# Kernel optimization log

Hardware: AMD Instinct MI355X
Metric: run time of the kernel (lower is better)

Reference implementation:

```python
import jax, jax.numpy as jnp
import numpy as np

N_NODES = 40000
N_EDGES = 300000
EMBED = 256
LN_EPS = 1e-5
LEAKY_SLOPE = 0.01


def setup_inputs() -> dict:
    key = jax.random.key(0)
    ks = jax.random.split(key, 5)
    H = jax.random.normal(ks[0], (N_NODES, EMBED), dtype=jnp.float32)
    E = jax.random.normal(ks[1], (N_EDGES, EMBED), dtype=jnp.float32)
    ht = jax.random.randint(ks[2], (N_EDGES, 2), 0, N_NODES, dtype=jnp.int64)
    # Linear weights in torch convention: [out_features, in_features]
    W_fwd = jax.random.normal(ks[3], (EMBED, 2 * EMBED), dtype=jnp.float32) * (1.0 / np.sqrt(2 * EMBED))
    W_back = jax.random.normal(ks[4], (EMBED, 2 * EMBED), dtype=jnp.float32) * (1.0 / np.sqrt(2 * EMBED))
    return {
        "H": H,
        "E": E,
        "ht": ht,
        "queries": jnp.zeros((1,), jnp.float32),            # unused (message_weighting_function=None)
        "influence_weights": jnp.zeros((1,), jnp.float32),  # modeled as None
        "W_fwd": W_fwd,
        "b_fwd": jnp.zeros((EMBED,), jnp.float32),
        "W_back": W_back,
        "b_back": jnp.zeros((EMBED,), jnp.float32),
        "ln_w": jnp.ones((EMBED,), jnp.float32),
        "ln_b": jnp.zeros((EMBED,), jnp.float32),
    }


def _layer_norm(x, w, b):
    mu = jnp.mean(x, axis=-1, keepdims=True)
    var = jnp.mean(jnp.square(x - mu), axis=-1, keepdims=True)  # biased, as torch LayerNorm
    return (x - mu) * jax.lax.rsqrt(var + LN_EPS) * w + b


def reference(H, E, ht, queries, influence_weights, W_fwd, b_fwd, W_back, b_back, ln_w, ln_b):
    # queries / influence_weights are None in the modeled configuration; ignored.
    heads = ht[:, 0]
    tails = ht[:, 1]
    n = H.shape[0]
    # gather -> concat -> linear (messages in both edge directions)
    msg_fwd = jnp.concatenate([H[heads], E], axis=1) @ W_fwd.T + b_fwd    # [m, d]
    msg_back = jnp.concatenate([H[tails], E], axis=1) @ W_back.T + b_back  # [m, d]
    # scatter-add aggregate: fwd messages go to tails, back messages to heads
    msg_dst = jnp.concatenate([tails, heads], axis=0)          # [2m]
    messages = jnp.concatenate([msg_fwd, msg_back], axis=0)    # [2m, d]
    agg = jax.ops.segment_sum(messages, msg_dst, num_segments=n)  # [n, d]
    counts = jax.ops.segment_sum(jnp.ones_like(msg_dst, dtype=H.dtype), msg_dst, num_segments=n)
    agg = agg / counts[:, None]
    out = _layer_norm(jax.nn.leaky_relu(agg, LEAKY_SLOPE) + H, ln_w, ln_b)
    return out
```

## Files before the change

kernel.cpp:

```cpp
#include <hip/hip_runtime.h>
#include <hip/hip_bf16.h>

#define N_NODES 40000
#define N_EDGES 300000
#define EMBED 256
#define CAP 64

typedef __attribute__((ext_vector_type(8))) short s16x8;
typedef __attribute__((ext_vector_type(4))) float f32x4;

__device__ __forceinline__ float b2f(unsigned short u) {
    union { unsigned int i; float f; } v; v.i = ((unsigned int)u) << 16; return v.f;
}
__device__ __forceinline__ unsigned short f2b(float f) {
    unsigned int x = __float_as_uint(f);
    x += 0x7fffu + ((x >> 16) & 1u);
    return (unsigned short)(x >> 16);
}
__device__ __forceinline__ bool ht_is_i64(const int* __restrict__ ht) {
    int o = 0;
    #pragma unroll
    for (int k = 1; k < 16; k += 2) o |= ht[k];
    return o == 0;
}
__device__ __forceinline__ int clampN(int v) {
    unsigned u = (unsigned)v;
    return (u < N_NODES) ? v : 0;
}

__global__ __launch_bounds__(256) void convert_kernel(
    const float* __restrict__ H, const float* __restrict__ Wf,
    const float* __restrict__ Wb,
    unsigned short* __restrict__ Hbf, unsigned short* __restrict__ Wcat)
{
    constexpr int NH4 = (N_NODES * EMBED) / 4;
    constexpr int NW4 = (EMBED * 2 * EMBED) / 4;
    int ci = blockIdx.x * 256 + threadIdx.x;
    const float* src; unsigned short* dst;
    if (ci < NH4) {
        src = &H[(size_t)ci * 4]; dst = &Hbf[(size_t)ci * 4];
    } else if (ci < NH4 + NW4) {
        int j = (ci - NH4) * 4; int n = j >> 9, k = j & 511;
        src = &Wf[j]; dst = &Wcat[(size_t)n * 1024 + k];
    } else if (ci < NH4 + 2 * NW4) {
        int j = (ci - NH4 - NW4) * 4; int n = j >> 9, k = j & 511;
        src = &Wb[j]; dst = &Wcat[(size_t)n * 1024 + 512 + k];
    } else return;
    float4 v = *(const float4*)src;
    ushort4 o; o.x = f2b(v.x); o.y = f2b(v.y); o.z = f2b(v.z); o.w = f2b(v.w);
    *(ushort4*)dst = o;
}

__global__ __launch_bounds__(256) void build_kernel(
    const int* __restrict__ ht,
    int* __restrict__ cntf, int* __restrict__ cntb,
    int* __restrict__ listf, int* __restrict__ listb)
{
    int e = blockIdx.x * 256 + threadIdx.x;
    if (e >= N_EDGES) return;
    const bool wide = ht_is_i64(ht);
    int head = clampN(wide ? ht[(size_t)4 * e]     : ht[2 * e]);
    int tail = clampN(wide ? ht[(size_t)4 * e + 2] : ht[2 * e + 1]);
    int pf = atomicAdd(&cntf[tail], 1);
    if (pf < CAP) listf[tail * CAP + pf] = e;
    int pb = atomicAdd(&cntb[head], 1);
    if (pb < CAP) listb[head * CAP + pb] = e;
}

__global__ __launch_bounds__(256, 4) void fused_kernel(
    const unsigned short* __restrict__ Hbf, const float* __restrict__ E,
    const int* __restrict__ ht, const unsigned short* __restrict__ Wcat,
    const float* __restrict__ bf_, const float* __restrict__ bb_,
    const float* __restrict__ H, const float* __restrict__ lw,
    const float* __restrict__ lb,
    const int* __restrict__ cntf, const int* __restrict__ cntb,
    const int* __restrict__ listf, const int* __restrict__ listb,
    float* __restrict__ out)
{
    constexpr int LDK = 1032;
    __shared__ unsigned short S[16 * LDK];
    __shared__ float stats[16][4][2];

    const int tid  = threadIdx.x;
    const int wid  = tid >> 6;
    const int lane = tid & 63;
    const int q    = lane >> 4;
    const int c    = lane & 15;
    const int m0   = blockIdx.x * 16;
    const bool wide = ht_is_i64(ht);

    int cF[4], cB[4];
    int eF[4], eB[4], nF[4], nB[4];
    #pragma unroll
    for (int i = 0; i < 4; i++) {
        const int node = m0 + wid * 4 + i;
        cF[i] = min(cntf[node], CAP);
        cB[i] = min(cntb[node], CAP);
    }
    #pragma unroll
    for (int i = 0; i < 4; i++) {
        const int node = m0 + wid * 4 + i;
        eF[i] = (lane < cF[i]) ? listf[node * CAP + lane] : 0;
        eB[i] = (lane < cB[i]) ? listb[node * CAP + lane] : 0;
    }
    #pragma unroll
    for (int i = 0; i < 4; i++) {
        nF[i] = clampN(wide ? ht[(size_t)4 * eF[i]]     : ht[2 * eF[i]]);
        nB[i] = clampN(wide ? ht[(size_t)4 * eB[i] + 2] : ht[2 * eB[i] + 1]);
    }

    const int loff = lane * 4;

    #pragma unroll
    for (int i = 0; i < 4; i++) {
        const int r = wid * 4 + i;
        float aHf[4] = {0.f,0.f,0.f,0.f}, aEf[4] = {0.f,0.f,0.f,0.f};
        float aHb[4] = {0.f,0.f,0.f,0.f}, aEb[4] = {0.f,0.f,0.f,0.f};

        for (int t = 0; t < cF[i]; t += 8) {
            float4 ev[8]; ushort4 hv[8]; float w[8];
            #pragma unroll
            for (int u = 0; u < 8; u++) {
                const int e  = __builtin_amdgcn_readlane(eF[i], t + u);
                const int nb = __builtin_amdgcn_readlane(nF[i], t + u);
                w[u] = (t + u < cF[i]) ? 1.0f : 0.0f;
                ev[u] = *(const float4*)(&E[(size_t)e * EMBED + loff]);
                hv[u] = *(const ushort4*)(&Hbf[(size_t)nb * EMBED + loff]);
            }
            #pragma unroll
            for (int u = 0; u < 8; u++) {
                aEf[0] += w[u] * ev[u].x; aEf[1] += w[u] * ev[u].y;
                aEf[2] += w[u] * ev[u].z; aEf[3] += w[u] * ev[u].w;
                aHf[0] += w[u] * b2f(hv[u].x); aHf[1] += w[u] * b2f(hv[u].y);
                aHf[2] += w[u] * b2f(hv[u].z); aHf[3] += w[u] * b2f(hv[u].w);
            }
        }
        for (int t = 0; t < cB[i]; t += 8) {
            float4 ev[8]; ushort4 hv[8]; float w[8];
            #pragma unroll
            for (int u = 0; u < 8; u++) {
                const int e  = __builtin_amdgcn_readlane(eB[i], t + u);
                const int nb = __builtin_amdgcn_readlane(nB[i], t + u);
                w[u] = (t + u < cB[i]) ? 1.0f : 0.0f;
                ev[u] = *(const float4*)(&E[(size_t)e * EMBED + loff]);
                hv[u] = *(const ushort4*)(&Hbf[(size_t)nb * EMBED + loff]);
            }
            #pragma unroll
            for (int u = 0; u < 8; u++) {
                aEb[0] += w[u] * ev[u].x; aEb[1] += w[u] * ev[u].y;
                aEb[2] += w[u] * ev[u].z; aEb[3] += w[u] * ev[u].w;
                aHb[0] += w[u] * b2f(hv[u].x); aHb[1] += w[u] * b2f(hv[u].y);
                aHb[2] += w[u] * b2f(hv[u].z); aHb[3] += w[u] * b2f(hv[u].w);
            }
        }

        ushort4 o;
        o.x=f2b(aHf[0]); o.y=f2b(aHf[1]); o.z=f2b(aHf[2]); o.w=f2b(aHf[3]);
        *(ushort4*)(&S[r * LDK +   0 + loff]) = o;
        o.x=f2b(aEf[0]); o.y=f2b(aEf[1]); o.z=f2b(aEf[2]); o.w=f2b(aEf[3]);
        *(ushort4*)(&S[r * LDK + 256 + loff]) = o;
        o.x=f2b(aHb[0]); o.y=f2b(aHb[1]); o.z=f2b(aHb[2]); o.w=f2b(aHb[3]);
        *(ushort4*)(&S[r * LDK + 512 + loff]) = o;
        o.x=f2b(aEb[0]); o.y=f2b(aEb[1]); o.z=f2b(aEb[2]); o.w=f2b(aEb[3]);
        *(ushort4*)(&S[r * LDK + 768 + loff]) = o;
    }
    __syncthreads();

    const int n0 = wid * 64;
    f32x4 acc[4];
    #pragma unroll
    for (int nt = 0; nt < 4; nt++) acc[nt] = (f32x4){0.f,0.f,0.f,0.f};

    #pragma unroll 4
    for (int k0 = 0; k0 < 1024; k0 += 32) {
        s16x8 a = *(const s16x8*)(&S[c * LDK + k0 + q * 8]);
        #pragma unroll
        for (int nt = 0; nt < 4; nt++) {
            s16x8 b = *(const s16x8*)(&Wcat[(size_t)(n0 + nt * 16 + c) * 1024 + k0 + q * 8]);
            acc[nt] = __builtin_amdgcn_mfma_f32_16x16x32_bf16(a, b, acc[nt], 0, 0, 0);
        }
    }

    float x[4][4];
    float sr[4], ssr[4];
    #pragma unroll
    for (int reg = 0; reg < 4; reg++) {
        const int row  = q * 4 + reg;
        const int node = m0 + row;
        const float cf = (float)cntf[node];
        const float cb = (float)cntb[node];
        const float tot = cf + cb;
        const float inv = (tot > 0.f) ? (1.0f / tot) : 0.f;
        float s = 0.f, ss = 0.f;
        #pragma unroll
        for (int nt = 0; nt < 4; nt++) {
            const int j = n0 + nt * 16 + c;
            float v = acc[nt][reg] + cf * bf_[j] + cb * bb_[j];
            float m = v * inv;
            m = (m > 0.f) ? m : 0.01f * m;
            float xx = m + H[(size_t)node * EMBED + j];
            x[reg][nt] = xx; s += xx; ss += xx * xx;
        }
        sr[reg] = s; ssr[reg] = ss;
    }
    #pragma unroll
    for (int off = 1; off < 16; off <<= 1) {
        #pragma unroll
        for (int reg = 0; reg < 4; reg++) {
            sr[reg]  += __shfl_xor(sr[reg],  off);
            ssr[reg] += __shfl_xor(ssr[reg], off);
        }
    }
    if (c == 0) {
        #pragma unroll
        for (int reg = 0; reg < 4; reg++) {
            stats[q * 4 + reg][wid][0] = sr[reg];
            stats[q * 4 + reg][wid][1] = ssr[reg];
        }
    }
    __syncthreads();
    #pragma unroll
    for (int reg = 0; reg < 4; reg++) {
        const int row  = q * 4 + reg;
        const int node = m0 + row;
        float s  = stats[row][0][0] + stats[row][1][0] + stats[row][2][0] + stats[row][3][0];
        float ss = stats[row][0][1] + stats[row][1][1] + stats[row][2][1] + stats[row][3][1];
        const float mean = s * (1.0f / EMBED);
        float var = ss * (1.0f / EMBED) - mean * mean;
        var = var < 0.f ? 0.f : var;
        const float rstd = rsqrtf(var + 1e-5f);
        #pragma unroll
        for (int nt = 0; nt < 4; nt++) {
            const int j = n0 + nt * 16 + c;
            out[(size_t)node * EMBED + j] = (x[reg][nt] - mean) * rstd * lw[j] + lb[j];
        }
    }
}

extern "C" void kernel_launch(void* const* d_in, const int* in_sizes, int n_in,
                              void* d_out, int out_size, void* d_ws, size_t ws_size,
                              hipStream_t stream) {
    const float* H   = (const float*)d_in[0];
    const float* E   = (const float*)d_in[1];
    const int*   ht  = (const int*)d_in[2];
    const float* Wf  = (const float*)d_in[5];
    const float* bf_ = (const float*)d_in[6];
    const float* Wb  = (const float*)d_in[7];
    const float* bb_ = (const float*)d_in[8];
    const float* lw  = (const float*)d_in[9];
    const float* lb  = (const float*)d_in[10];
    float* out = (float*)d_out;

    int* cntf  = (int*)d_ws;
    int* cntb  = cntf + 40960;
    int* listf = cntb + 40960;
    int* listb = listf + N_NODES * CAP;
    unsigned short* Hbf  = (unsigned short*)(listb + N_NODES * CAP);
    unsigned short* Wcat = Hbf + (size_t)N_NODES * EMBED;

    hipMemsetAsync(d_ws, 0, 2 * 40960 * sizeof(int), stream);

    constexpr int NCHUNK = (N_NODES * EMBED + 2 * EMBED * 2 * EMBED) / 4;
    convert_kernel<<<(NCHUNK + 255) / 256, 256, 0, stream>>>(H, Wf, Wb, Hbf, Wcat);
    build_kernel<<<(N_EDGES + 255) / 256, 256, 0, stream>>>(ht, cntf, cntb, listf, listb);
    fused_kernel<<<N_NODES / 16, 256, 0, stream>>>(Hbf, E, ht, Wcat, bf_, bb_,
                                                   H, lw, lb, cntf, cntb,
                                                   listf, listb, out);
}
```

Before: 687.4 us.

## Convert E to fp16 and interleave forward/backward edge gathers with manual waitcnt

When the workspace is large enough, the convert kernel now also writes an fp16 copy of the edge features E. The fused kernel then gathers half the bytes per edge row. The per-node gather is restructured to issue forward and backward loads together via inline asm, with explicit vmcnt waits, to raise memory-level parallelism, and launch bounds drop to 2 waves per SIMD. The trade-off is an extra full streaming pass over E every call, plus reduced precision for the E sum.

```diff
diff --git a/kernel.cpp b/kernel.cpp
--- a/kernel.cpp
+++ b/kernel.cpp
@@ -1,5 +1,6 @@
 #include <hip/hip_runtime.h>
 #include <hip/hip_bf16.h>
+#include <hip/hip_fp16.h>
 
 #define N_NODES 40000
 #define N_EDGES 300000
@@ -8,10 +9,8 @@
 
 typedef __attribute__((ext_vector_type(8))) short s16x8;
 typedef __attribute__((ext_vector_type(4))) float f32x4;
-
-__device__ __forceinline__ float b2f(unsigned short u) {
-    union { unsigned int i; float f; } v; v.i = ((unsigned int)u) << 16; return v.f;
-}
+typedef __attribute__((ext_vector_type(2))) unsigned int u32x2;
+
 __device__ __forceinline__ unsigned short f2b(float f) {
     unsigned int x = __float_as_uint(f);
     x += 0x7fffu + ((x >> 16) & 1u);
@@ -28,27 +27,45 @@
     return (u < N_NODES) ? v : 0;
 }
 
+template<bool EF16> struct EVT;
+template<> struct EVT<true>  { using T = u32x2; };
+template<> struct EVT<false> { using T = f32x4; };
+
+template<bool EF16>
 __global__ __launch_bounds__(256) void convert_kernel(
     const float* __restrict__ H, const float* __restrict__ Wf,
-    const float* __restrict__ Wb,
-    unsigned short* __restrict__ Hbf, unsigned short* __restrict__ Wcat)
+    const float* __restrict__ Wb, const float* __restrict__ E,
+    unsigned short* __restrict__ Hbf, unsigned short* __restrict__ Wcat,
+    unsigned short* __restrict__ Ef)
 {
     constexpr int NH4 = (N_NODES * EMBED) / 4;
     constexpr int NW4 = (EMBED * 2 * EMBED) / 4;
+    constexpr int NE4 = (N_EDGES * EMBED) / 4;
     int ci = blockIdx.x * 256 + threadIdx.x;
-    const float* src; unsigned short* dst;
     if (ci < NH4) {
-        src = &H[(size_t)ci * 4]; dst = &Hbf[(size_t)ci * 4];
+        float4 v = *(const float4*)&H[(size_t)ci * 4];
+        ushort4 o; o.x=f2b(v.x); o.y=f2b(v.y); o.z=f2b(v.z); o.w=f2b(v.w);
+        *(ushort4*)&Hbf[(size_t)ci * 4] = o;
     } else if (ci < NH4 + NW4) {
         int j = (ci - NH4) * 4; int n = j >> 9, k = j & 511;
-        src = &Wf[j]; dst = &Wcat[(size_t)n * 1024 + k];
+        float4 v = *(const float4*)&Wf[j];
+        ushort4 o; o.x=f2b(v.x); o.y=f2b(v.y); o.z=f2b(v.z); o.w=f2b(v.w);
+        *(ushort4*)&Wcat[(size_t)n * 1024 + k] = o;
     } else if (ci < NH4 + 2 * NW4) {
         int j = (ci - NH4 - NW4) * 4; int n = j >> 9, k = j & 511;
-        src = &Wb[j]; dst = &Wcat[(size_t)n * 1024 + 512 + k];
-    } else return;
-    float4 v = *(const float4*)src;
-    ushort4 o; o.x = f2b(v.x); o.y = f2b(v.y); o.z = f2b(v.z); o.w = f2b(v.w);
-    *(ushort4*)dst = o;
+        float4 v = *(const float4*)&Wb[j];
+        ushort4 o; o.x=f2b(v.x); o.y=f2b(v.y); o.z=f2b(v.z); o.w=f2b(v.w);
+        *(ushort4*)&Wcat[(size_t)n * 1024 + 512 + k] = o;
+    } else if (EF16 && ci < NH4 + 2 * NW4 + NE4) {
+        size_t j = (size_t)(ci - NH4 - 2 * NW4) * 4;
+        float4 v = *(const float4*)&E[j];
+        ushort4 o;
+        o.x = __half_as_ushort(__float2half(v.x));
+        o.y = __half_as_ushort(__float2half(v.y));
+        o.z = __half_as_ushort(__float2half(v.z));
+        o.w = __half_as_ushort(__float2half(v.w));
+        *(ushort4*)&Ef[j] = o;
+    }
 }
 
 __global__ __launch_bounds__(256) void build_kernel(
@@ -67,8 +84,88 @@
     if (pb < CAP) listb[head * CAP + pb] = e;
 }
 
-__global__ __launch_bounds__(256, 4) void fused_kernel(
-    const unsigned short* __restrict__ Hbf, const float* __restrict__ E,
+template<bool EF16>
+__device__ __forceinline__ void gather_node(
+    const void* __restrict__ Ep, const unsigned short* __restrict__ Hbf,
+    int eFr, int nFr, int eBr, int nBr, int ncF, int ncB, int lane,
+    float (&aHf)[4], float (&aEf)[4], float (&aHb)[4], float (&aEb)[4])
+{
+    using EV = typename EVT<EF16>::T;
+    const int nmax = (ncF > ncB) ? ncF : ncB;
+    for (int t = 0; t < nmax; t += 8) {
+        EV evf[8], evb[8]; u32x2 hvf[8], hvb[8];
+        #pragma unroll
+        for (int u = 0; u < 8; u++) {
+            const int e_  = __builtin_amdgcn_readlane(eFr, t + u);
+            const int nb_ = __builtin_amdgcn_readlane(nFr, t + u);
+            const unsigned short* ph = Hbf + (size_t)nb_ * EMBED + lane * 4;
+            if constexpr (EF16) {
+                const unsigned short* pe = (const unsigned short*)Ep + (size_t)e_ * EMBED + lane * 4;
+                asm volatile("global_load_dwordx2 %0, %1, off" : "=v"(evf[u]) : "v"(pe));
+            } else {
+                const float* pe = (const float*)Ep + (size_t)e_ * EMBED + lane * 4;
+                asm volatile("global_load_dwordx4 %0, %1, off" : "=v"(evf[u]) : "v"(pe));
+            }
+            asm volatile("global_load_dwordx2 %0, %1, off" : "=v"(hvf[u]) : "v"(ph));
+        }
+        #pragma unroll
+        for (int u = 0; u < 8; u++) {
+            const int e_  = __builtin_amdgcn_readlane(eBr, t + u);
+            const int nb_ = __builtin_amdgcn_readlane(nBr, t + u);
+            const unsigned short* ph = Hbf + (size_t)nb_ * EMBED + lane * 4;
+            if constexpr (EF16) {
+                const unsigned short* pe = (const unsigned short*)Ep + (size_t)e_ * EMBED + lane * 4;
+                asm volatile("global_load_dwordx2 %0, %1, off" : "=v"(evb[u]) : "v"(pe));
+            } else {
+                const float* pe = (const float*)Ep + (size_t)e_ * EMBED + lane * 4;
+                asm volatile("global_load_dwordx4 %0, %1, off" : "=v"(evb[u]) : "v"(pe));
+            }
+            asm volatile("global_load_dwordx2 %0, %1, off" : "=v"(hvb[u]) : "v"(ph));
+        }
+        asm volatile("s_waitcnt vmcnt(16)" ::: "memory");
+        __builtin_amdgcn_sched_barrier(0);
+        #pragma unroll
+        for (int u = 0; u < 8; u++) {
+            const float w = (t + u < ncF) ? 1.0f : 0.0f;
+            if constexpr (EF16) {
+                aEf[0] += w * __half2float(__ushort_as_half((unsigned short)(evf[u].x & 0xffffu)));
+                aEf[1] += w * __half2float(__ushort_as_half((unsigned short)(evf[u].x >> 16)));
+                aEf[2] += w * __half2float(__ushort_as_half((unsigned short)(evf[u].y & 0xffffu)));
+                aEf[3] += w * __half2float(__ushort_as_half((unsigned short)(evf[u].y >> 16)));
+            } else {
+                aEf[0] += w * evf[u].x; aEf[1] += w * evf[u].y;
+                aEf[2] += w * evf[u].z; aEf[3] += w * evf[u].w;
+            }
+            aHf[0] += w * __uint_as_float(hvf[u].x << 16);
+            aHf[1] += w * __uint_as_float(hvf[u].x & 0xffff0000u);
+            aHf[2] += w * __uint_as_float(hvf[u].y << 16);
+            aHf[3] += w * __uint_as_float(hvf[u].y & 0xffff0000u);
+        }
+        asm volatile("s_waitcnt vmcnt(0)" ::: "memory");
+        __builtin_amdgcn_sched_barrier(0);
+        #pragma unroll
+        for (int u = 0; u < 8; u++) {
+            const float w = (t + u < ncB) ? 1.0f : 0.0f;
+            if constexpr (EF16) {
+                aEb[0] += w * __half2float(__ushort_as_half((unsigned short)(evb[u].x & 0xffffu)));
+                aEb[1] += w * __half2float(__ushort_as_half((unsigned short)(evb[u].x >> 16)));
+                aEb[2] += w * __half2float(__ushort_as_half((unsigned short)(evb[u].y & 0xffffu)));
+                aEb[3] += w * __half2float(__ushort_as_half((unsigned short)(evb[u].y >> 16)));
+            } else {
+                aEb[0] += w * evb[u].x; aEb[1] += w * evb[u].y;
+                aEb[2] += w * evb[u].z; aEb[3] += w * evb[u].w;
+            }
+            aHb[0] += w * __uint_as_float(hvb[u].x << 16);
+            aHb[1] += w * __uint_as_float(hvb[u].x & 0xffff0000u);
+            aHb[2] += w * __uint_as_float(hvb[u].y << 16);
+            aHb[3] += w * __uint_as_float(hvb[u].y & 0xffff0000u);
+        }
+    }
+}
+
+template<bool EF16>
+__global__ __launch_bounds__(256, 2) void fused_kernel(
+    const unsigned short* __restrict__ Hbf, const void* __restrict__ Ep,
     const int* __restrict__ ht, const unsigned short* __restrict__ Wcat,
     const float* __restrict__ bf_, const float* __restrict__ bb_,
     const float* __restrict__ H, const float* __restrict__ lw,
@@ -117,42 +214,10 @@
         float aHf[4] = {0.f,0.f,0.f,0.f}, aEf[4] = {0.f,0.f,0.f,0.f};
         float aHb[4] = {0.f,0.f,0.f,0.f}, aEb[4] = {0.f,0.f,0.f,0.f};
 
-        for (int t = 0; t < cF[i]; t += 8) {
-            float4 ev[8]; ushort4 hv[8]; float w[8];
-            #pragma unroll
-            for (int u = 0; u < 8; u++) {
-                const int e  = __builtin_amdgcn_readlane(eF[i], t + u);
-                const int nb = __builtin_amdgcn_readlane(nF[i], t + u);
-                w[u] = (t + u < cF[i]) ? 1.0f : 0.0f;
-                ev[u] = *(const float4*)(&E[(size_t)e * EMBED + loff]);
-                hv[u] = *(const ushort4*)(&Hbf[(size_t)nb * EMBED + loff]);
-            }
-            #pragma unroll
-            for (int u = 0; u < 8; u++) {
-                aEf[0] += w[u] * ev[u].x; aEf[1] += w[u] * ev[u].y;
-                aEf[2] += w[u] * ev[u].z; aEf[3] += w[u] * ev[u].w;
-                aHf[0] += w[u] * b2f(hv[u].x); aHf[1] += w[u] * b2f(hv[u].y);
-                aHf[2] += w[u] * b2f(hv[u].z); aHf[3] += w[u] * b2f(hv[u].w);
-            }
-        }
-        for (int t = 0; t < cB[i]; t += 8) {
-            float4 ev[8]; ushort4 hv[8]; float w[8];
-            #pragma unroll
-            for (int u = 0; u < 8; u++) {
-                const int e  = __builtin_amdgcn_readlane(eB[i], t + u);
-                const int nb = __builtin_amdgcn_readlane(nB[i], t + u);
-                w[u] = (t + u < cB[i]) ? 1.0f : 0.0f;
-                ev[u] = *(const float4*)(&E[(size_t)e * EMBED + loff]);
-                hv[u] = *(const ushort4*)(&Hbf[(size_t)nb * EMBED + loff]);
-            }
-            #pragma unroll
-            for (int u = 0; u < 8; u++) {
-                aEb[0] += w[u] * ev[u].x; aEb[1] += w[u] * ev[u].y;
-                aEb[2] += w[u] * ev[u].z; aEb[3] += w[u] * ev[u].w;
-                aHb[0] += w[u] * b2f(hv[u].x); aHb[1] += w[u] * b2f(hv[u].y);
-                aHb[2] += w[u] * b2f(hv[u].z); aHb[3] += w[u] * b2f(hv[u].w);
-            }
-        }
+        const int ncF = __builtin_amdgcn_readfirstlane(cF[i]);
+        const int ncB = __builtin_amdgcn_readfirstlane(cB[i]);
+        gather_node<EF16>(Ep, Hbf, eF[i], nF[i], eB[i], nB[i], ncF, ncB, lane,
+                          aHf, aEf, aHb, aEb);
 
         ushort4 o;
         o.x=f2b(aHf[0]); o.y=f2b(aHf[1]); o.z=f2b(aHf[2]); o.w=f2b(aHf[3]);
@@ -257,13 +322,32 @@
     int* listb = listf + N_NODES * CAP;
     unsigned short* Hbf  = (unsigned short*)(listb + N_NODES * CAP);
     unsigned short* Wcat = Hbf + (size_t)N_NODES * EMBED;
+    unsigned short* Ef   = Wcat + (size_t)256 * 1024;
+
+    const size_t need_base = (size_t)(2 * 40960) * 4 + (size_t)2 * N_NODES * CAP * 4
+                           + ((size_t)N_NODES * EMBED + (size_t)256 * 1024) * 2;
+    const size_t need_ef16 = need_base + (size_t)N_EDGES * EMBED * 2;
+    const bool ef16 = (ws_size >= need_ef16);
 
     hipMemsetAsync(d_ws, 0, 2 * 40960 * sizeof(int), stream);
 
-    constexpr int NCHUNK = (N_NODES * EMBED + 2 * EMBED * 2 * EMBED) / 4;
-    convert_kernel<<<(NCHUNK + 255) / 256, 256, 0, stream>>>(H, Wf, Wb, Hbf, Wcat);
+    constexpr int NBASE = (N_NODES * EMBED + 2 * EMBED * 2 * EMBED) / 4;
+    constexpr int NEXT  = NBASE + (N_EDGES * EMBED) / 4;
+    if (ef16) {
+        convert_kernel<true><<<(NEXT + 255) / 256, 256, 0, stream>>>(
+            H, Wf, Wb, E, Hbf, Wcat, Ef);
+    } else {
+        convert_kernel<false><<<(NBASE + 255) / 256, 256, 0, stream>>>(
+            H, Wf, Wb, E, Hbf, Wcat, Ef);
+    }
     build_kernel<<<(N_EDGES + 255) / 256, 256, 0, stream>>>(ht, cntf, cntb, listf, listb);
-    fused_kernel<<<N_NODES / 16, 256, 0, stream>>>(Hbf, E, ht, Wcat, bf_, bb_,
-                                                   H, lw, lb, cntf, cntb,
-                                                   listf, listb, out);
-}
+    if (ef16) {
+        fused_kernel<true><<<N_NODES / 16, 256, 0, stream>>>(
+            Hbf, (const void*)Ef, ht, Wcat, bf_, bb_, H, lw, lb,
+            cntf, cntb, listf, listb, out);
+    } else {
+        fused_kernel<false><<<N_NODES / 16, 256, 0, stream>>>(
+            Hbf, (const void*)E, ht, Wcat, bf_, bb_, H, lw, lb,
+            cntf, cntb, listf, listb, out);
+    }
+}
```

New measurement: 731.3 us. +6.4%, slower.

## Build CSR with prefix sum and pre-permuted fp16 edge features for contiguous gathers

Applied to the files above, without the earlier changes.

Replaces the capped per-node edge lists with a CSR built from count, prefix-scan and permute kernels. The permute kernel writes E converted to fp16 twice, once in forward-destination order and once in backward-destination order, so the fused kernel reads edge features contiguously and at half width instead of gathering fp32 rows at random. This costs an extra pass over E, two 150MB-scale fp16 writes, and a serial single-block prefix scan per direction. Launch bounds drop to 2 waves per SIMD, and the old path is kept as a fallback when the workspace is too small.

```diff
diff --git a/kernel.cpp b/kernel.cpp
--- a/kernel.cpp
+++ b/kernel.cpp
@@ -1,5 +1,6 @@
 #include <hip/hip_runtime.h>
 #include <hip/hip_bf16.h>
+#include <hip/hip_fp16.h>
 
 #define N_NODES 40000
 #define N_EDGES 300000
@@ -8,6 +9,7 @@
 
 typedef __attribute__((ext_vector_type(8))) short s16x8;
 typedef __attribute__((ext_vector_type(4))) float f32x4;
+typedef __attribute__((ext_vector_type(2))) unsigned int u32x2;
 
 __device__ __forceinline__ float b2f(unsigned short u) {
     union { unsigned int i; float f; } v; v.i = ((unsigned int)u) << 16; return v.f;
@@ -51,6 +53,251 @@
     *(ushort4*)dst = o;
 }
 
+__global__ __launch_bounds__(256) void count_kernel(
+    const int* __restrict__ ht, int* __restrict__ cntf, int* __restrict__ cntb)
+{
+    int e = blockIdx.x * 256 + threadIdx.x;
+    if (e >= N_EDGES) return;
+    const bool wide = ht_is_i64(ht);
+    int head = clampN(wide ? ht[(size_t)4 * e]     : ht[2 * e]);
+    int tail = clampN(wide ? ht[(size_t)4 * e + 2] : ht[2 * e + 1]);
+    atomicAdd(&cntf[tail], 1);
+    atomicAdd(&cntb[head], 1);
+}
+
+__global__ __launch_bounds__(256) void prefix_kernel(
+    const int* __restrict__ cntf, const int* __restrict__ cntb,
+    int* __restrict__ offsf, int* __restrict__ offsb)
+{
+    const int* cnt = (blockIdx.x == 0) ? cntf : cntb;
+    int* offs      = (blockIdx.x == 0) ? offsf : offsb;
+    __shared__ int buf[256];
+    const int tid = threadIdx.x;
+    int carry = 0;
+    for (int base = 0; base < N_NODES; base += 256) {
+        const int i = base + tid;
+        const int v = (i < N_NODES) ? cnt[i] : 0;
+        buf[tid] = v;
+        __syncthreads();
+        for (int off = 1; off < 256; off <<= 1) {
+            int t = (tid >= off) ? buf[tid - off] : 0;
+            __syncthreads();
+            buf[tid] += t;
+            __syncthreads();
+        }
+        if (i < N_NODES) offs[i] = carry + buf[tid] - v;
+        carry += buf[255];
+        __syncthreads();
+    }
+}
+
+__global__ __launch_bounds__(256) void permute_kernel(
+    const float* __restrict__ E, const int* __restrict__ ht,
+    const int* __restrict__ offsf, const int* __restrict__ offsb,
+    int* __restrict__ fillf, int* __restrict__ fillb,
+    unsigned short* __restrict__ Epf, unsigned short* __restrict__ Epb,
+    int* __restrict__ nbrf, int* __restrict__ nbrb)
+{
+    const int e = blockIdx.x * 4 + (threadIdx.x >> 6);
+    if (e >= N_EDGES) return;
+    const int lane = threadIdx.x & 63;
+    const bool wide = ht_is_i64(ht);
+    const int head = clampN(wide ? ht[(size_t)4 * e]     : ht[2 * e]);
+    const int tail = clampN(wide ? ht[(size_t)4 * e + 2] : ht[2 * e + 1]);
+    int pf = 0, pb = 0;
+    if (lane == 0) {
+        pf = atomicAdd(&fillf[tail], 1);
+        pb = atomicAdd(&fillb[head], 1);
+    }
+    pf = __shfl(pf, 0); pb = __shfl(pb, 0);
+    const int sf = offsf[tail] + pf;
+    const int sb = offsb[head] + pb;
+    if (lane == 0) { nbrf[sf] = head; nbrb[sb] = tail; }
+    float4 v = *(const float4*)&E[(size_t)e * EMBED + lane * 4];
+    ushort4 o;
+    o.x = __half_as_ushort(__float2half(v.x));
+    o.y = __half_as_ushort(__float2half(v.y));
+    o.z = __half_as_ushort(__float2half(v.z));
+    o.w = __half_as_ushort(__float2half(v.w));
+    *(ushort4*)&Epf[(size_t)sf * EMBED + lane * 4] = o;
+    *(ushort4*)&Epb[(size_t)sb * EMBED + lane * 4] = o;
+}
+
+__global__ __launch_bounds__(256, 2) void csr_fused_kernel(
+    const unsigned short* __restrict__ Hbf,
+    const unsigned short* __restrict__ Epf, const unsigned short* __restrict__ Epb,
+    const unsigned short* __restrict__ Wcat,
+    const float* __restrict__ bf_, const float* __restrict__ bb_,
+    const float* __restrict__ H, const float* __restrict__ lw,
+    const float* __restrict__ lb,
+    const int* __restrict__ cntf, const int* __restrict__ cntb,
+    const int* __restrict__ offsf, const int* __restrict__ offsb,
+    const int* __restrict__ nbrf, const int* __restrict__ nbrb,
+    float* __restrict__ out)
+{
+    constexpr int LDK = 1032;
+    __shared__ unsigned short S[16 * LDK];
+    __shared__ float stats[16][4][2];
+
+    const int tid  = threadIdx.x;
+    const int wid  = tid >> 6;
+    const int lane = tid & 63;
+    const int q    = lane >> 4;
+    const int c    = lane & 15;
+    const int m0   = blockIdx.x * 16;
+    const int loff = lane * 4;
+
+    int cF[4], cB[4], oF[4], oB[4], nF[4], nB[4];
+    #pragma unroll
+    for (int i = 0; i < 4; i++) {
+        const int node = m0 + wid * 4 + i;
+        cF[i] = min(cntf[node], CAP);
+        cB[i] = min(cntb[node], CAP);
+        oF[i] = offsf[node];
+        oB[i] = offsb[node];
+    }
+    #pragma unroll
+    for (int i = 0; i < 4; i++) {
+        nF[i] = (lane < cF[i]) ? nbrf[oF[i] + lane] : 0;
+        nB[i] = (lane < cB[i]) ? nbrb[oB[i] + lane] : 0;
+    }
+
+    #pragma unroll
+    for (int i = 0; i < 4; i++) {
+        const int r = wid * 4 + i;
+        float aHf[4] = {0,0,0,0}, aEf[4] = {0,0,0,0};
+        float aHb[4] = {0,0,0,0}, aEb[4] = {0,0,0,0};
+
+        const int ncF = __builtin_amdgcn_readfirstlane(cF[i]);
+        const int obF = __builtin_amdgcn_readfirstlane(oF[i]);
+        for (int t = 0; t < ncF; t += 8) {
+            u32x2 ev[8], hv[8];
+            #pragma unroll
+            for (int u = 0; u < 8; u++) {
+                ev[u] = *(const u32x2*)(&Epf[(size_t)(obF + t + u) * EMBED + loff]);
+                const int nb = __builtin_amdgcn_readlane(nF[i], t + u);
+                hv[u] = *(const u32x2*)(&Hbf[(size_t)nb * EMBED + loff]);
+            }
+            #pragma unroll
+            for (int u = 0; u < 8; u++) {
+                const float w = (t + u < ncF) ? 1.0f : 0.0f;
+                aEf[0] += w * __half2float(__ushort_as_half((unsigned short)(ev[u].x & 0xffffu)));
+                aEf[1] += w * __half2float(__ushort_as_half((unsigned short)(ev[u].x >> 16)));
+                aEf[2] += w * __half2float(__ushort_as_half((unsigned short)(ev[u].y & 0xffffu)));
+                aEf[3] += w * __half2float(__ushort_as_half((unsigned short)(ev[u].y >> 16)));
+                aHf[0] += w * __uint_as_float(hv[u].x << 16);
+                aHf[1] += w * __uint_as_float(hv[u].x & 0xffff0000u);
+                aHf[2] += w * __uint_as_float(hv[u].y << 16);
+                aHf[3] += w * __uint_as_float(hv[u].y & 0xffff0000u);
+            }
+        }
+        const int ncB = __builtin_amdgcn_readfirstlane(cB[i]);
+        const int obB = __builtin_amdgcn_readfirstlane(oB[i]);
+        for (int t = 0; t < ncB; t += 8) {
+            u32x2 ev[8], hv[8];
+            #pragma unroll
+            for (int u = 0; u < 8; u++) {
+                ev[u] = *(const u32x2*)(&Epb[(size_t)(obB + t + u) * EMBED + loff]);
+                const int nb = __builtin_amdgcn_readlane(nB[i], t + u);
+                hv[u] = *(const u32x2*)(&Hbf[(size_t)nb * EMBED + loff]);
+            }
+            #pragma unroll
+            for (int u = 0; u < 8; u++) {
+                const float w = (t + u < ncB) ? 1.0f : 0.0f;
+                aEb[0] += w * __half2float(__ushort_as_half((unsigned short)(ev[u].x & 0xffffu)));
+                aEb[1] += w * __half2float(__ushort_as_half((unsigned short)(ev[u].x >> 16)));
+                aEb[2] += w * __half2float(__ushort_as_half((unsigned short)(ev[u].y & 0xffffu)));
+                aEb[3] += w * __half2float(__ushort_as_half((unsigned short)(ev[u].y >> 16)));
+                aHb[0] += w * __uint_as_float(hv[u].x << 16);
+                aHb[1] += w * __uint_as_float(hv[u].x & 0xffff0000u);
+                aHb[2] += w * __uint_as_float(hv[u].y << 16);
+                aHb[3] += w * __uint_as_float(hv[u].y & 0xffff0000u);
+            }
+        }
+
+        ushort4 o;
+        o.x=f2b(aHf[0]); o.y=f2b(aHf[1]); o.z=f2b(aHf[2]); o.w=f2b(aHf[3]);
+        *(ushort4*)(&S[r * LDK +   0 + loff]) = o;
+        o.x=f2b(aEf[0]); o.y=f2b(aEf[1]); o.z=f2b(aEf[2]); o.w=f2b(aEf[3]);
+        *(ushort4*)(&S[r * LDK + 256 + loff]) = o;
+        o.x=f2b(aHb[0]); o.y=f2b(aHb[1]); o.z=f2b(aHb[2]); o.w=f2b(aHb[3]);
+        *(ushort4*)(&S[r * LDK + 512 + loff]) = o;
+        o.x=f2b(aEb[0]); o.y=f2b(aEb[1]); o.z=f2b(aEb[2]); o.w=f2b(aEb[3]);
+        *(ushort4*)(&S[r * LDK + 768 + loff]) = o;
+    }
+    __syncthreads();
+
+    const int n0 = wid * 64;
+    f32x4 acc[4];
+    #pragma unroll
+    for (int nt = 0; nt < 4; nt++) acc[nt] = (f32x4){0.f,0.f,0.f,0.f};
+
+    #pragma unroll 4
+    for (int k0 = 0; k0 < 1024; k0 += 32) {
+        s16x8 a = *(const s16x8*)(&S[c * LDK + k0 + q * 8]);
+        #pragma unroll
+        for (int nt = 0; nt < 4; nt++) {
+            s16x8 b = *(const s16x8*)(&Wcat[(size_t)(n0 + nt * 16 + c) * 1024 + k0 + q * 8]);
+            acc[nt] = __builtin_amdgcn_mfma_f32_16x16x32_bf16(a, b, acc[nt], 0, 0, 0);
+        }
+    }
+
+    float x[4][4];
+    float sr[4], ssr[4];
+    #pragma unroll
+    for (int reg = 0; reg < 4; reg++) {
+        const int row  = q * 4 + reg;
+        const int node = m0 + row;
+        const float cf = (float)cntf[node];
+        const float cb = (float)cntb[node];
+        const float tot = cf + cb;
+        const float inv = (tot > 0.f) ? (1.0f / tot) : 0.f;
+        float s = 0.f, ss = 0.f;
+        #pragma unroll
+        for (int nt = 0; nt < 4; nt++) {
+            const int j = n0 + nt * 16 + c;
+            float v = acc[nt][reg] + cf * bf_[j] + cb * bb_[j];
+            float m = v * inv;
+            m = (m > 0.f) ? m : 0.01f * m;
+            float xx = m + H[(size_t)node * EMBED + j];
+            x[reg][nt] = xx; s += xx; ss += xx * xx;
+        }
+        sr[reg] = s; ssr[reg] = ss;
+    }
+    #pragma unroll
+    for (int off = 1; off < 16; off <<= 1) {
+        #pragma unroll
+        for (int reg = 0; reg < 4; reg++) {
+            sr[reg]  += __shfl_xor(sr[reg],  off);
+            ssr[reg] += __shfl_xor(ssr[reg], off);
+        }
+    }
+    if (c == 0) {
+        #pragma unroll
+        for (int reg = 0; reg < 4; reg++) {
+            stats[q * 4 + reg][wid][0] = sr[reg];
+            stats[q * 4 + reg][wid][1] = ssr[reg];
+        }
+    }
+    __syncthreads();
+    #pragma unroll
+    for (int reg = 0; reg < 4; reg++) {
+        const int row  = q * 4 + reg;
+        const int node = m0 + row;
+        float s  = stats[row][0][0] + stats[row][1][0] + stats[row][2][0] + stats[row][3][0];
+        float ss = stats[row][0][1] + stats[row][1][1] + stats[row][2][1] + stats[row][3][1];
+        const float mean = s * (1.0f / EMBED);
+        float var = ss * (1.0f / EMBED) - mean * mean;
+        var = var < 0.f ? 0.f : var;
+        const float rstd = rsqrtf(var + 1e-5f);
+        #pragma unroll
+        for (int nt = 0; nt < 4; nt++) {
+            const int j = n0 + nt * 16 + c;
+            out[(size_t)node * EMBED + j] = (x[reg][nt] - mean) * rstd * lw[j] + lb[j];
+        }
+    }
+}
+
 __global__ __launch_bounds__(256) void build_kernel(
     const int* __restrict__ ht,
     int* __restrict__ cntf, int* __restrict__ cntb,
@@ -67,7 +314,7 @@
     if (pb < CAP) listb[head * CAP + pb] = e;
 }
 
-__global__ __launch_bounds__(256, 4) void fused_kernel(
+__global__ __launch_bounds__(256, 2) void gather_fused_kernel(
     const unsigned short* __restrict__ Hbf, const float* __restrict__ E,
     const int* __restrict__ ht, const unsigned short* __restrict__ Wcat,
     const float* __restrict__ bf_, const float* __restrict__ bb_,
@@ -110,12 +357,11 @@
     }
 
     const int loff = lane * 4;
-
     #pragma unroll
     for (int i = 0; i < 4; i++) {
         const int r = wid * 4 + i;
-        float aHf[4] = {0.f,0.f,0.f,0.f}, aEf[4] = {0.f,0.f,0.f,0.f};
-        float aHb[4] = {0.f,0.f,0.f,0.f}, aEb[4] = {0.f,0.f,0.f,0.f};
+        float aHf[4] = {0,0,0,0}, aEf[4] = {0,0,0,0};
+        float aHb[4] = {0,0,0,0}, aEb[4] = {0,0,0,0};
 
         for (int t = 0; t < cF[i]; t += 8) {
             float4 ev[8]; ushort4 hv[8]; float w[8];
@@ -153,7 +399,6 @@
                 aHb[2] += w[u] * b2f(hv[u].z); aHb[3] += w[u] * b2f(hv[u].w);
             }
         }
-
         ushort4 o;
         o.x=f2b(aHf[0]); o.y=f2b(aHf[1]); o.z=f2b(aHf[2]); o.w=f2b(aHf[3]);
         *(ushort4*)(&S[r * LDK +   0 + loff]) = o;
@@ -170,7 +415,6 @@
     f32x4 acc[4];
     #pragma unroll
     for (int nt = 0; nt < 4; nt++) acc[nt] = (f32x4){0.f,0.f,0.f,0.f};
-
     #pragma unroll 4
     for (int k0 = 0; k0 < 1024; k0 += 32) {
         s16x8 a = *(const s16x8*)(&S[c * LDK + k0 + q * 8]);
@@ -251,19 +495,50 @@
     const float* lb  = (const float*)d_in[10];
     float* out = (float*)d_out;
 
-    int* cntf  = (int*)d_ws;
-    int* cntb  = cntf + 40960;
-    int* listf = cntb + 40960;
-    int* listb = listf + N_NODES * CAP;
-    unsigned short* Hbf  = (unsigned short*)(listb + N_NODES * CAP);
-    unsigned short* Wcat = Hbf + (size_t)N_NODES * EMBED;
-
-    hipMemsetAsync(d_ws, 0, 2 * 40960 * sizeof(int), stream);
-
-    constexpr int NCHUNK = (N_NODES * EMBED + 2 * EMBED * 2 * EMBED) / 4;
-    convert_kernel<<<(NCHUNK + 255) / 256, 256, 0, stream>>>(H, Wf, Wb, Hbf, Wcat);
-    build_kernel<<<(N_EDGES + 255) / 256, 256, 0, stream>>>(ht, cntf, cntb, listf, listb);
-    fused_kernel<<<N_NODES / 16, 256, 0, stream>>>(Hbf, E, ht, Wcat, bf_, bb_,
-                                                   H, lw, lb, cntf, cntb,
-                                                   listf, listb, out);
-}
+    constexpr size_t NBPAD = N_EDGES + 64;
+    const size_t need_csr = (size_t)(6 * 40960) * 4 + (size_t)2 * 300032 * 4
+        + ((size_t)N_NODES * EMBED + (size_t)256 * 1024 + 2 * NBPAD * EMBED) * 2;
+
+    if (ws_size >= need_csr) {
+        int* cntf  = (int*)d_ws;
+        int* cntb  = cntf + 40960;
+        int* fillf = cntb + 40960;
+        int* fillb = fillf + 40960;
+        int* offsf = fillb + 40960;
+        int* offsb = offsf + 40960;
+        int* nbrf  = offsb + 40960;
+        int* nbrb  = nbrf + 300032;
+        unsigned short* Hbf  = (unsigned short*)(nbrb + 300032);
+        unsigned short* Wcat = Hbf + (size_t)N_NODES * EMBED;
+        unsigned short* Epf  = Wcat + (size_t)256 * 1024;
+        unsigned short* Epb  = Epf + NBPAD * EMBED;
+
+        hipMemsetAsync(d_ws, 0, 4 * 40960 * sizeof(int), stream);
+
+        constexpr int NCHUNK = (N_NODES * EMBED + 2 * EMBED * 2 * EMBED) / 4;
+        convert_kernel<<<(NCHUNK + 255) / 256, 256, 0, stream>>>(H, Wf, Wb, Hbf, Wcat);
+        count_kernel<<<(N_EDGES + 255) / 256, 256, 0, stream>>>(ht, cntf, cntb);
+        prefix_kernel<<<2, 256, 0, stream>>>(cntf, cntb, offsf, offsb);
+        permute_kernel<<<(N_EDGES + 3) / 4, 256, 0, stream>>>(
+            E, ht, offsf, offsb, fillf, fillb, Epf, Epb, nbrf, nbrb);
+        csr_fused_kernel<<<N_NODES / 16, 256, 0, stream>>>(
+            Hbf, Epf, Epb, Wcat, bf_, bb_, H, lw, lb,
+            cntf, cntb, offsf, offsb, nbrf, nbrb, out);
+    } else {
+        int* cntf  = (int*)d_ws;
+        int* cntb  = cntf + 40960;
+        int* listf = cntb + 40960;
+        int* listb = listf + N_NODES * CAP;
+        unsigned short* Hbf  = (unsigned short*)(listb + N_NODES * CAP);
+        unsigned short* Wcat = Hbf + (size_t)N_NODES * EMBED;
+
+        hipMemsetAsync(d_ws, 0, 2 * 40960 * sizeof(int), stream);
+
+        constexpr int NCHUNK = (N_NODES * EMBED + 2 * EMBED * 2 * EMBED) / 4;
+        convert_kernel<<<(NCHUNK + 255) / 256, 256, 0, stream>>>(H, Wf, Wb, Hbf, Wcat);
+        build_kernel<<<(N_EDGES + 255) / 256, 256, 0, stream>>>(ht, cntf, cntb, listf, listb);
+        gather_fused_kernel<<<N_NODES / 16, 256, 0, stream>>>(Hbf, E, ht, Wcat, bf_, bb_,
+                                                              H, lw, lb, cntf, cntb,
+                                                              listf, listb, out);
+    }
+}
```

New measurement: 938.0 us. 1.36x slower.
